# Optimization experiments

Measured on AMD Instinct MI355X. Metric: run time of the kernel, lower is better.

The kernel has to match this reference:

```python
import jax, jax.numpy as jnp
import numpy as np

EMB = 512
HID = 1024
BATCH = 64
SEQ = 512


def setup_inputs() -> dict:
    key = jax.random.key(0)
    k1, k2, k3 = jax.random.split(key, 3)
    X = jax.random.normal(k1, (BATCH, SEQ, EMB), dtype=jnp.float32)
    # nn.Linear weights are [out, in]; scaled like torch default init
    W_ax = jax.random.normal(k2, (HID, EMB), dtype=jnp.float32) / np.sqrt(EMB)
    W_aa = jax.random.normal(k3, (HID, HID), dtype=jnp.float32) / np.sqrt(HID)
    b_a = jnp.ones((HID,), dtype=jnp.float32)
    return {"X": X, "W_ax": W_ax, "W_aa": W_aa, "b_a": b_a}


def reference(X, W_ax, W_aa, b_a):
    # X: [B, S, E] -> time-major [S, B, E]
    Xt = jnp.transpose(X, (1, 0, 2))
    # Precompute input projections for all timesteps in one big GEMM: [S, B, H]
    xproj = jnp.einsum('sbe,he->sbh', Xt, W_ax) + b_a
    a0 = jnp.zeros((X.shape[0], HID), dtype=X.dtype)

    def step(a, xp):
        a_n = jnp.tanh(xp + a @ W_aa.T)
        return a_n, a_n

    hidden, outputs = jax.lax.scan(step, a0, xproj)
    return outputs, hidden  # outputs: [S, B, H], hidden: [B, H]
```

## Files before the change

### kernel.cpp

```cpp
#include <hip/hip_runtime.h>
#include <hip/hip_fp16.h>
#include <hip/hip_cooperative_groups.h>

typedef _Float16 f16;
typedef _Float16 half8 __attribute__((ext_vector_type(8)));
typedef _Float16 f16x4 __attribute__((ext_vector_type(4)));
typedef float floatx4 __attribute__((ext_vector_type(4)));
typedef unsigned long long u64;

#define BATCH 64
#define SEQ 512
#define EMB 512
#define HID 1024
#define GWG 8

#define ABUF_HALFS 131072
#define BAR_OFF 2359296

__global__ __launch_bounds__(256) void k0_cvt_waa(const float* __restrict__ W,
                                                  f16* __restrict__ W16,
                                                  f16* __restrict__ abuf,
                                                  unsigned* __restrict__ bar) {
    int gtid = blockIdx.x * 256 + threadIdx.x;
    int i = gtid * 4;
    float4 v = *(const float4*)(W + i);
    f16x4 h;
    h[0] = (f16)v.x; h[1] = (f16)v.y; h[2] = (f16)v.z; h[3] = (f16)v.w;
    *(f16x4*)(W16 + i) = h;
    if (gtid < 32768) {
        int g = gtid >> 13, off = gtid & 8191;
        ((unsigned*)abuf)[g * 16384 + off] = 0u;
    }
    if (gtid < 4) bar[gtid * 64] = 0u;
}

__global__ __launch_bounds__(256) void k1_xproj(const float* __restrict__ X,
                                                const float* __restrict__ Wax,
                                                const float* __restrict__ ba,
                                                float* __restrict__ out) {
    __shared__ __align__(16) f16 Xhi[64][40];
    __shared__ __align__(16) f16 Xlo[64][40];
    __shared__ __align__(16) f16 Wh[64][40];
    const int tid  = threadIdx.x;
    const int lane = tid & 63;
    const int wave = tid >> 6;
    const int vm = wave >> 1, vn = wave & 1;
    const int m0 = blockIdx.x * 64;
    const int n0 = blockIdx.y * 64;
    const int q = lane >> 4, c = lane & 15;
    const int srow = tid >> 2, scol = (tid & 3) * 8;

    floatx4 acc[2][2] = {};

    for (int kc = 0; kc < EMB; kc += 32) {
        const float* xp = X + (size_t)(m0 + srow) * EMB + kc + scol;
        float4 x0 = *(const float4*)xp;
        float4 x1 = *(const float4*)(xp + 4);
        float xv[8] = {x0.x, x0.y, x0.z, x0.w, x1.x, x1.y, x1.z, x1.w};
        half8 xh, xl;
#pragma unroll
        for (int j = 0; j < 8; j++) {
            f16 h = (f16)xv[j];
            xh[j] = h;
            xl[j] = (f16)(xv[j] - (float)h);
        }
        *(half8*)&Xhi[srow][scol] = xh;
        *(half8*)&Xlo[srow][scol] = xl;
        const float* wp = Wax + (size_t)(n0 + srow) * EMB + kc + scol;
        float4 w0 = *(const float4*)wp;
        float4 w1 = *(const float4*)(wp + 4);
        float wv[8] = {w0.x, w0.y, w0.z, w0.w, w1.x, w1.y, w1.z, w1.w};
        half8 wh8;
#pragma unroll
        for (int j = 0; j < 8; j++) wh8[j] = (f16)wv[j];
        *(half8*)&Wh[srow][scol] = wh8;
        __syncthreads();

#pragma unroll
        for (int im = 0; im < 2; im++) {
            half8 ahi = *(const half8*)&Xhi[vm * 32 + im * 16 + c][q * 8];
            half8 alo = *(const half8*)&Xlo[vm * 32 + im * 16 + c][q * 8];
#pragma unroll
            for (int in = 0; in < 2; in++) {
                half8 bf = *(const half8*)&Wh[vn * 32 + in * 16 + c][q * 8];
                acc[im][in] = __builtin_amdgcn_mfma_f32_16x16x32_f16(ahi, bf, acc[im][in], 0, 0, 0);
                acc[im][in] = __builtin_amdgcn_mfma_f32_16x16x32_f16(alo, bf, acc[im][in], 0, 0, 0);
            }
        }
        __syncthreads();
    }
#pragma unroll
    for (int im = 0; im < 2; im++) {
#pragma unroll
        for (int in = 0; in < 2; in++) {
            int n = n0 + vn * 32 + in * 16 + c;
            float bias = ba[n];
#pragma unroll
            for (int r = 0; r < 4; r++) {
                int m = m0 + vm * 32 + im * 16 + q * 4 + r;
                int b = m >> 9, s = m & 511;
                out[(size_t)(s * BATCH + b) * HID + n] = acc[im][in][r] + bias;
            }
        }
    }
}

__global__ __launch_bounds__(512, 1) void k2_scan(const f16* __restrict__ W16,
                                                  float* __restrict__ out,
                                                  f16* __restrict__ abuf,
                                                  unsigned* __restrict__ bar) {
    __shared__ __align__(16) f16 S[16][1032];
    const int tid  = threadIdx.x;
    const int lane = tid & 63;
    const int wave = tid >> 6;
    const int grp  = blockIdx.x >> 3;
    const int wig  = ((blockIdx.x & 7) << 3) + wave;
    const int j0   = wig << 4;
    const int b0   = grp << 4;
    const int q = lane >> 4, c = lane & 15;

    half8 w[32];
    {
        const f16* Wrow = W16 + (size_t)(j0 + c) * HID + q * 8;
#pragma unroll
        for (int t = 0; t < 32; t++) w[t] = *(const half8*)(Wrow + t * 32);
    }
    unsigned* cnt = bar + grp * 64;
    f16* const buf0 = abuf + (size_t)grp * 32768;
    f16* const buf1 = buf0 + 16384;

    for (int s = 0; s < SEQ; s++) {
        const f16* src = (s & 1) ? buf1 : buf0;
        f16* dst       = (s & 1) ? buf0 : buf1;
        const int b = b0 + c;
        size_t obase = ((size_t)s * BATCH + b) * HID + j0 + (q << 2);
        float4 xp = *(const float4*)(out + obase);
        if (tid == 0) {
            unsigned tgt = (unsigned)(GWG * s);
            while (__hip_atomic_load(cnt, __ATOMIC_RELAXED, __HIP_MEMORY_SCOPE_AGENT) < tgt) {}
        }
        __syncthreads();
        {
            u64 tmp[8];
#pragma unroll
            for (int it = 0; it < 8; it++)
                tmp[it] = __hip_atomic_load((const u64*)(src + (it * 512 + tid) * 4),
                                            __ATOMIC_RELAXED, __HIP_MEMORY_SCOPE_AGENT);
#pragma unroll
            for (int it = 0; it < 8; it++) {
                int idx = (it * 512 + tid) * 4;
                *(u64*)&S[idx >> 10][idx & 1023] = tmp[it];
            }
        }
        __syncthreads();
        floatx4 acc = {0.f, 0.f, 0.f, 0.f};
#pragma unroll
        for (int t = 0; t < 32; t++) {
            half8 bfrag = *(const half8*)&S[c][t * 32 + q * 8];
            acc = __builtin_amdgcn_mfma_f32_16x16x32_f16(w[t], bfrag, acc, 0, 0, 0);
        }
        float4 v;
        v.x = tanhf(xp.x + acc[0]);
        v.y = tanhf(xp.y + acc[1]);
        v.z = tanhf(xp.z + acc[2]);
        v.w = tanhf(xp.w + acc[3]);
        *(float4*)(out + obase) = v;
        union { f16x4 h; u64 u; } cv;
        cv.h[0] = (f16)v.x; cv.h[1] = (f16)v.y; cv.h[2] = (f16)v.z; cv.h[3] = (f16)v.w;
        __hip_atomic_store((u64*)(dst + c * 1024 + j0 + (q << 2)), cv.u,
                           __ATOMIC_RELAXED, __HIP_MEMORY_SCOPE_AGENT);
        if (s == SEQ - 1)
            *(float4*)(out + (size_t)SEQ * BATCH * HID + (size_t)b * HID + j0 + (q << 2)) = v;
        asm volatile("s_waitcnt vmcnt(0)" ::: "memory");
        __syncthreads();
        if (tid == 0)
            __hip_atomic_fetch_add(cnt, 1u, __ATOMIC_RELAXED, __HIP_MEMORY_SCOPE_AGENT);
    }
}

extern "C" void kernel_launch(void* const* d_in, const int* in_sizes, int n_in,
                              void* d_out, int out_size, void* d_ws, size_t ws_size,
                              hipStream_t stream) {
    const float* X   = (const float*)d_in[0];
    const float* Wax = (const float*)d_in[1];
    const float* Waa = (const float*)d_in[2];
    const float* ba  = (const float*)d_in[3];
    float* out = (float*)d_out;

    f16* abuf = (f16*)d_ws;
    f16* W16  = abuf + ABUF_HALFS;
    unsigned* bar = (unsigned*)((char*)d_ws + BAR_OFF);

    k0_cvt_waa<<<dim3(HID * HID / 1024), dim3(256), 0, stream>>>(Waa, W16, abuf, bar);
    k1_xproj<<<dim3((BATCH * SEQ) / 64, HID / 64), dim3(256), 0, stream>>>(X, Wax, ba, out);

    void* args[] = {(void*)&W16, (void*)&out, (void*)&abuf, (void*)&bar};
    hipLaunchCooperativeKernel((void*)k2_scan, dim3(32), dim3(512), args, 0, stream);
}
```

Baseline: 2.200 ms.

## Split each batch group into two interleaved half-batch chains with separate barriers

Each 16-batch group is divided into two 8-batch chains, each with its own activation plane and arrival counter, and the block alternates between them every timestep. The aim is to let one chain's cross-block barrier wait overlap with progress on the other chain. The output stores are also moved after the counter increment to shorten the critical path. In exchange, every step now runs two full MFMA passes and two barrier round trips, with half of the lanes' results discarded each time.

```diff
diff --git a/kernel.cpp b/kernel.cpp
--- a/kernel.cpp
+++ b/kernel.cpp
@@ -28,10 +28,10 @@
     h[0] = (f16)v.x; h[1] = (f16)v.y; h[2] = (f16)v.z; h[3] = (f16)v.w;
     *(f16x4*)(W16 + i) = h;
     if (gtid < 32768) {
-        int g = gtid >> 13, off = gtid & 8191;
-        ((unsigned*)abuf)[g * 16384 + off] = 0u;
-    }
-    if (gtid < 4) bar[gtid * 64] = 0u;
+        int pid = gtid >> 12, off = gtid & 4095;
+        ((unsigned*)abuf)[pid * 8192 + off] = 0u;
+    }
+    if (gtid < 8) bar[gtid * 64] = 0u;
 }
 
 __global__ __launch_bounds__(256) void k1_xproj(const float* __restrict__ X,
@@ -118,6 +118,9 @@
     const int j0   = wig << 4;
     const int b0   = grp << 4;
     const int q = lane >> 4, c = lane & 15;
+    const int myChain = c >> 3;
+    const int cc = c & 7;
+    const int b = b0 + c;
 
     half8 w[32];
     {
@@ -125,56 +128,69 @@
 #pragma unroll
         for (int t = 0; t < 32; t++) w[t] = *(const half8*)(Wrow + t * 32);
     }
-    unsigned* cnt = bar + grp * 64;
-    f16* const buf0 = abuf + (size_t)grp * 32768;
-    f16* const buf1 = buf0 + 16384;
+    unsigned* const cnt0 = bar + (grp * 2 + 0) * 64;
+    unsigned* const cnt1 = bar + (grp * 2 + 1) * 64;
+    f16* const plane0 = abuf + (size_t)(grp * 2 + 0) * 16384;
+    f16* const plane1 = abuf + (size_t)(grp * 2 + 1) * 16384;
 
     for (int s = 0; s < SEQ; s++) {
-        const f16* src = (s & 1) ? buf1 : buf0;
-        f16* dst       = (s & 1) ? buf0 : buf1;
-        const int b = b0 + c;
-        size_t obase = ((size_t)s * BATCH + b) * HID + j0 + (q << 2);
-        float4 xp = *(const float4*)(out + obase);
-        if (tid == 0) {
-            unsigned tgt = (unsigned)(GWG * s);
-            while (__hip_atomic_load(cnt, __ATOMIC_RELAXED, __HIP_MEMORY_SCOPE_AGENT) < tgt) {}
-        }
-        __syncthreads();
-        {
-            u64 tmp[8];
-#pragma unroll
-            for (int it = 0; it < 8; it++)
-                tmp[it] = __hip_atomic_load((const u64*)(src + (it * 512 + tid) * 4),
-                                            __ATOMIC_RELAXED, __HIP_MEMORY_SCOPE_AGENT);
-#pragma unroll
-            for (int it = 0; it < 8; it++) {
-                int idx = (it * 512 + tid) * 4;
-                *(u64*)&S[idx >> 10][idx & 1023] = tmp[it];
-            }
-        }
-        __syncthreads();
-        floatx4 acc = {0.f, 0.f, 0.f, 0.f};
-#pragma unroll
-        for (int t = 0; t < 32; t++) {
-            half8 bfrag = *(const half8*)&S[c][t * 32 + q * 8];
-            acc = __builtin_amdgcn_mfma_f32_16x16x32_f16(w[t], bfrag, acc, 0, 0, 0);
-        }
-        float4 v;
-        v.x = tanhf(xp.x + acc[0]);
-        v.y = tanhf(xp.y + acc[1]);
-        v.z = tanhf(xp.z + acc[2]);
-        v.w = tanhf(xp.w + acc[3]);
-        *(float4*)(out + obase) = v;
-        union { f16x4 h; u64 u; } cv;
-        cv.h[0] = (f16)v.x; cv.h[1] = (f16)v.y; cv.h[2] = (f16)v.z; cv.h[3] = (f16)v.w;
-        __hip_atomic_store((u64*)(dst + c * 1024 + j0 + (q << 2)), cv.u,
-                           __ATOMIC_RELAXED, __HIP_MEMORY_SCOPE_AGENT);
-        if (s == SEQ - 1)
-            *(float4*)(out + (size_t)SEQ * BATCH * HID + (size_t)b * HID + j0 + (q << 2)) = v;
-        asm volatile("s_waitcnt vmcnt(0)" ::: "memory");
-        __syncthreads();
-        if (tid == 0)
-            __hip_atomic_fetch_add(cnt, 1u, __ATOMIC_RELAXED, __HIP_MEMORY_SCOPE_AGENT);
+#pragma unroll
+        for (int h = 0; h < 2; h++) {
+            unsigned* const cnt = h ? cnt1 : cnt0;
+            f16* const plane   = h ? plane1 : plane0;
+            const f16* src = plane + ((s & 1) ? 8192 : 0);
+            f16* dst       = plane + ((s & 1) ? 0 : 8192);
+            const bool act = (myChain == h);
+            const size_t obase = ((size_t)s * BATCH + b) * HID + j0 + (q << 2);
+            float4 xp;
+            if (act) xp = *(const float4*)(out + obase);
+            if (tid == 0) {
+                const unsigned tgt = (unsigned)(GWG * s);
+                while (__hip_atomic_load(cnt, __ATOMIC_RELAXED,
+                                         __HIP_MEMORY_SCOPE_AGENT) < tgt) {}
+            }
+            __syncthreads();
+            {
+                u64 tmp[4];
+#pragma unroll
+                for (int it = 0; it < 4; it++)
+                    tmp[it] = __hip_atomic_load((const u64*)(src + (it * 512 + tid) * 4),
+                                                __ATOMIC_RELAXED, __HIP_MEMORY_SCOPE_AGENT);
+#pragma unroll
+                for (int it = 0; it < 4; it++) {
+                    int idx = (it * 512 + tid) * 4;
+                    *(u64*)&S[(h << 3) + (idx >> 10)][idx & 1023] = tmp[it];
+                }
+            }
+            __syncthreads();
+            floatx4 acc = {0.f, 0.f, 0.f, 0.f};
+#pragma unroll
+            for (int t = 0; t < 32; t++) {
+                half8 bfrag = *(const half8*)&S[c][t * 32 + q * 8];
+                acc = __builtin_amdgcn_mfma_f32_16x16x32_f16(w[t], bfrag, acc, 0, 0, 0);
+            }
+            float4 v;
+            if (act) {
+                v.x = tanhf(xp.x + acc[0]);
+                v.y = tanhf(xp.y + acc[1]);
+                v.z = tanhf(xp.z + acc[2]);
+                v.w = tanhf(xp.w + acc[3]);
+                union { f16x4 h4; u64 u; } cv;
+                cv.h4[0] = (f16)v.x; cv.h4[1] = (f16)v.y;
+                cv.h4[2] = (f16)v.z; cv.h4[3] = (f16)v.w;
+                __hip_atomic_store((u64*)(dst + cc * 1024 + j0 + (q << 2)), cv.u,
+                                   __ATOMIC_RELAXED, __HIP_MEMORY_SCOPE_AGENT);
+            }
+            asm volatile("s_waitcnt vmcnt(0)" ::: "memory");
+            __syncthreads();
+            if (tid == 0)
+                __hip_atomic_fetch_add(cnt, 1u, __ATOMIC_RELAXED, __HIP_MEMORY_SCOPE_AGENT);
+            if (act) {
+                *(float4*)(out + obase) = v;
+                if (s == SEQ - 1)
+                    *(float4*)(out + (size_t)SEQ * BATCH * HID + (size_t)b * HID + j0 + (q << 2)) = v;
+            }
+        }
     }
 }
 
```

Measured after the change: 3.317 ms. 50.8% more time.
